# Optimization experiments

Hardware: AMD Instinct MI355X
Metric: run time of the kernel (lower is better)

## Reference

```python
import jax, jax.numpy as jnp
import numpy as np

ITERATIONS = 3
OUT_CAPS, OUT_DIM = 10, 16


def squash(x):
    # square_norm / (1 + square_norm) * x / (sqrt(square_norm) + 1e-6), norm over last axis
    sn = jnp.sum(x * x, axis=-1, keepdims=True)
    return sn / (1.0 + sn) * x / (jnp.sqrt(sn) + 1e-6)


def setup_inputs() -> dict:
    key = jax.random.key(0)
    kx, kw = jax.random.split(key)
    x = jax.random.normal(kx, (256, 32, 6, 6, 8), dtype=jnp.float32)
    W = 0.01 * jax.random.normal(kw, (1, 32, 6, 6, 10, 8, 16), dtype=jnp.float32)
    return {"x": x, "W": W}


def reference(x, W):
    w = W[0]  # [i,j,k,o,d,e]
    # u_hat: prediction vectors, [B, i, j, k, O, E]
    u_hat = jnp.einsum('bijkd,ijkode->bijkoe', x, w)
    u_det = jax.lax.stop_gradient(u_hat)
    b = jnp.zeros(u_hat.shape[:-1], dtype=u_hat.dtype)  # [B,i,j,k,O]
    for _ in range(ITERATIONS - 1):
        c = jax.nn.softmax(b, axis=-1)
        s = jnp.einsum('bijko,bijkoe->boe', c, u_det)   # reduce over all input-capsule axes
        v = squash(s)                                    # [B,O,E]
        b = b + jnp.einsum('bijkoe,boe->bijko', u_det, v)
    c = jax.nn.softmax(b, axis=-1)
    s = jnp.einsum('bijko,bijkoe->boe', c, u_hat)
    v = squash(s)
    return v.reshape(-1, OUT_CAPS, OUT_DIM)
```

## Files before the change

### kernel.cpp

```cpp
#include <hip/hip_runtime.h>
#include <math.h>

#define BATCH 256
#define IC    1152
#define DD    8
#define OO    10
#define EE    16
#define BTILE 64
#define NBT   4
#define NT    256
#define CHUNK 6
#define NCHUNK 192
#define WPC   1280
#define WHALF ((size_t)IC * 160 * 8)

typedef __attribute__((ext_vector_type(8))) short short8;
typedef __attribute__((ext_vector_type(4))) float f32x4;

__device__ __forceinline__ unsigned short f2bf(float f) {
    unsigned u = __float_as_uint(f);
    unsigned r = u + 0x7FFFu + ((u >> 16) & 1u);
    return (unsigned short)(r >> 16);
}
__device__ __forceinline__ float bf2f(unsigned short h) {
    return __uint_as_float(((unsigned)h) << 16);
}

__global__ __launch_bounds__(256) void caps_prep_kernel(
    const float* __restrict__ W,
    unsigned short* __restrict__ w_hi,
    unsigned short* __restrict__ w_lo)
{
    const int idx = blockIdx.x * 256 + threadIdx.x;
    const int ijk = idx / 160;
    const int oe  = idx - ijk * 160;
    const int o = oe >> 4, e = oe & 15;
    const float* src = W + (size_t)ijk * WPC + o * 128 + e;
    short8 hv, lv;
    #pragma unroll
    for (int d = 0; d < 8; ++d) {
        const float f = src[d * 16];
        const unsigned short h = f2bf(f);
        hv[d] = (short)h;
        lv[d] = (short)f2bf(f - bf2f(h));
    }
    *reinterpret_cast<short8*>(w_hi + (size_t)idx * 8) = hv;
    *reinterpret_cast<short8*>(w_lo + (size_t)idx * 8) = lv;
}

__global__ __launch_bounds__(NT) void caps_pass_kernel(
    const float* __restrict__ x,
    const unsigned short* __restrict__ w_hi,
    const unsigned short* __restrict__ w_lo,
    const float* __restrict__ V,
    float* __restrict__ s_part,
    int first)
{
    __shared__ unsigned short wl_hi[CHUNK * 160 * 8];
    __shared__ unsigned short wl_lo[CHUNK * 160 * 8];
    __shared__ unsigned short x_hi[CHUNK][BTILE][8];
    __shared__ unsigned short x_lo[CHUNK][BTILE][8];
    __shared__ unsigned short zpad[8];

    const int tid  = threadIdx.x;
    const int wv   = tid >> 6;
    const int lane = tid & 63;
    const int q    = lane >> 4;
    const int em   = lane & 15;
    const int ijk0 = blockIdx.x * CHUNK;
    const int bg0  = blockIdx.y * BTILE;

    if (tid < 8) zpad[tid] = 0;

    {
        const float4* sh = reinterpret_cast<const float4*>(w_hi + (size_t)ijk0 * 160 * 8);
        const float4* sl = reinterpret_cast<const float4*>(w_lo + (size_t)ijk0 * 160 * 8);
        float4* dh = reinterpret_cast<float4*>(wl_hi);
        float4* dl = reinterpret_cast<float4*>(wl_lo);
        #pragma unroll
        for (int i = 0; i < 4; ++i) {
            const int f = tid + i * NT;
            if (f < CHUNK * 160) { dh[f] = sh[f]; dl[f] = sl[f]; }
        }
    }
    {
        #pragma unroll
        for (int i = 0; i < 2; ++i) {
            const int u = tid + i * NT;
            if (u < CHUNK * BTILE) {
                const int b = u / CHUNK, s = u - b * CHUNK;
                const float* xp = x + ((size_t)(bg0 + b) * IC + (ijk0 + s)) * DD;
                const float4 xa = *reinterpret_cast<const float4*>(xp);
                const float4 xb = *reinterpret_cast<const float4*>(xp + 4);
                const float vv[8] = {xa.x,xa.y,xa.z,xa.w, xb.x,xb.y,xb.z,xb.w};
                short8 hv, lv;
                #pragma unroll
                for (int j = 0; j < 8; ++j) {
                    const unsigned short h = f2bf(vv[j]);
                    hv[j] = (short)h;
                    lv[j] = (short)f2bf(vv[j] - bf2f(h));
                }
                *reinterpret_cast<short8*>(&x_hi[s][b][0]) = hv;
                *reinterpret_cast<short8*>(&x_lo[s][b][0]) = lv;
            }
        }
    }

    f32x4 vreg[OO];
    const int b = bg0 + 16 * wv + em;
    if (!first) {
        #pragma unroll
        for (int o = 0; o < OO; ++o) {
            const float4 t = *reinterpret_cast<const float4*>(
                V + (size_t)b * (OO * EE) + o * EE + 4 * q);
            vreg[o] = (f32x4){t.x, t.y, t.z, t.w};
        }
    }
    __syncthreads();

    const unsigned short* wbase = (q == 1) ? wl_lo : ((q == 3) ? zpad : wl_hi);
    const unsigned short* xbase = (q == 2) ? &x_lo[0][0][0]
                                : ((q == 3) ? zpad : &x_hi[0][0][0]);
    const int msk = (q == 3) ? 0 : 1;

    f32x4 sacc[OO];
    #pragma unroll
    for (int o = 0; o < OO; ++o) sacc[o] = (f32x4){0.f, 0.f, 0.f, 0.f};

    #pragma unroll 1
    for (int s = 0; s < CHUNK; ++s) {
        const short8 xf = *reinterpret_cast<const short8*>(
            xbase + msk * ((s * BTILE + 16 * wv + em) * 8));
        f32x4 u[OO];
        #pragma unroll
        for (int o = 0; o < OO; ++o) {
            const short8 wf = *reinterpret_cast<const short8*>(
                wbase + msk * ((s * 160 + o * 16 + em) * 8));
            u[o] = __builtin_amdgcn_mfma_f32_16x16x32_bf16(
                       wf, xf, (f32x4){0.f, 0.f, 0.f, 0.f}, 0, 0, 0);
        }
        if (!first) {
            float elg[OO];
            float den = 0.f;
            #pragma unroll
            for (int o = 0; o < OO; ++o) {
                float t = u[o][0]*vreg[o][0] + u[o][1]*vreg[o][1]
                        + u[o][2]*vreg[o][2] + u[o][3]*vreg[o][3];
                t += __shfl_xor(t, 16);
                t += __shfl_xor(t, 32);
                elg[o] = __expf(t);
                den += elg[o];
            }
            const float rden = __fdividef(1.0f, den);
            #pragma unroll
            for (int o = 0; o < OO; ++o)
                sacc[o] += u[o] * (elg[o] * rden);
        } else {
            #pragma unroll
            for (int o = 0; o < OO; ++o) sacc[o] += u[o];
        }
    }

    {
        const float mul = first ? 0.1f : 1.0f;
        float* sp = s_part + (((size_t)blockIdx.x * BATCH + b) * OO) * EE + 4 * q;
        #pragma unroll
        for (int o = 0; o < OO; ++o) {
            const f32x4 t = sacc[o];
            float4 w4;
            w4.x = mul * t[0]; w4.y = mul * t[1];
            w4.z = mul * t[2]; w4.w = mul * t[3];
            *reinterpret_cast<float4*>(sp + o * EE) = w4;
        }
    }
}

__global__ __launch_bounds__(1024) void caps_squash_kernel(
    const float* __restrict__ s_part,
    float* __restrict__ V,
    float* __restrict__ out,
    int accum, int last)
{
    __shared__ float red[15][64];
    const int lane = threadIdx.x & 63;
    const int w    = threadIdx.x >> 6;
    const int g    = blockIdx.x * 64 + lane;

    const float* sp = s_part + g;
    float s = 0.f;
    #pragma unroll
    for (int i = 0; i < NCHUNK / 16; ++i)
        s += sp[(size_t)(w * (NCHUNK / 16) + i) * (BATCH * OO * EE)];

    if (w > 0) red[w - 1][lane] = s;
    __syncthreads();
    if (w == 0) {
        #pragma unroll
        for (int i = 0; i < 15; ++i) s += red[i][lane];

        float sq = s * s;
        #pragma unroll
        for (int m = 1; m < 16; m <<= 1) sq += __shfl_xor(sq, m, 16);

        const float scale = sq / (1.f + sq) / (sqrtf(sq) + 1e-6f);
        const float v = scale * s;

        if (last)       out[g] = v;
        else if (accum) V[g]  += v;
        else            V[g]   = v;
    }
}

extern "C" void kernel_launch(void* const* d_in, const int* in_sizes, int n_in,
                              void* d_out, int out_size, void* d_ws, size_t ws_size,
                              hipStream_t stream) {
    const float* x = (const float*)d_in[0];
    const float* W = (const float*)d_in[1];
    float* out = (float*)d_out;

    float* s_part = (float*)d_ws;
    float* V      = s_part + (size_t)NCHUNK * BATCH * OO * EE;
    unsigned short* w_hi = (unsigned short*)(V + BATCH * OO * EE);
    unsigned short* w_lo = w_hi + WHALF;

    dim3 grid(NCHUNK, NBT), blk(NT);
    const int sq_blocks = (BATCH * OO * EE) / 64;

    caps_prep_kernel<<<(IC * 160) / 256, 256, 0, stream>>>(W, w_hi, w_lo);

    caps_pass_kernel<<<grid, blk, 0, stream>>>(x, w_hi, w_lo, V, s_part, 1);
    caps_squash_kernel<<<sq_blocks, 1024, 0, stream>>>(s_part, V, out, 0, 0);
    caps_pass_kernel<<<grid, blk, 0, stream>>>(x, w_hi, w_lo, V, s_part, 0);
    caps_squash_kernel<<<sq_blocks, 1024, 0, stream>>>(s_part, V, out, 1, 0);
    caps_pass_kernel<<<grid, blk, 0, stream>>>(x, w_hi, w_lo, V, s_part, 0);
    caps_squash_kernel<<<sq_blocks, 1024, 0, stream>>>(s_part, V, out, 0, 1);
}
```

Measured before the change: 152.8 us.

## Recompute MFMA predictions instead of holding them; shrink chunk to four capsules

The routing pass no longer keeps all ten u vectors live across the softmax. It recomputes each MFMA product in a second loop, with an opaque copy of the LDS base pointer so the compiler cannot merge the two loads. This cuts register pressure in exchange for twice the MFMA and LDS reads. The input-capsule chunk shrinks from 6 to 4, which gives more blocks, lets the x staging use one element per thread, and shrinks LDS per block, but adds more partial sums for the squash kernel to reduce.

```diff
diff --git a/kernel.cpp b/kernel.cpp
--- a/kernel.cpp
+++ b/kernel.cpp
@@ -9,8 +9,8 @@
 #define BTILE 64
 #define NBT   4
 #define NT    256
-#define CHUNK 6
-#define NCHUNK 192
+#define CHUNK 4
+#define NCHUNK 288
 #define WPC   1280
 #define WHALF ((size_t)IC * 160 * 8)
 
@@ -78,32 +78,26 @@
         float4* dh = reinterpret_cast<float4*>(wl_hi);
         float4* dl = reinterpret_cast<float4*>(wl_lo);
         #pragma unroll
-        for (int i = 0; i < 4; ++i) {
+        for (int i = 0; i < 3; ++i) {
             const int f = tid + i * NT;
             if (f < CHUNK * 160) { dh[f] = sh[f]; dl[f] = sl[f]; }
         }
     }
     {
-        #pragma unroll
-        for (int i = 0; i < 2; ++i) {
-            const int u = tid + i * NT;
-            if (u < CHUNK * BTILE) {
-                const int b = u / CHUNK, s = u - b * CHUNK;
-                const float* xp = x + ((size_t)(bg0 + b) * IC + (ijk0 + s)) * DD;
-                const float4 xa = *reinterpret_cast<const float4*>(xp);
-                const float4 xb = *reinterpret_cast<const float4*>(xp + 4);
-                const float vv[8] = {xa.x,xa.y,xa.z,xa.w, xb.x,xb.y,xb.z,xb.w};
-                short8 hv, lv;
-                #pragma unroll
-                for (int j = 0; j < 8; ++j) {
-                    const unsigned short h = f2bf(vv[j]);
-                    hv[j] = (short)h;
-                    lv[j] = (short)f2bf(vv[j] - bf2f(h));
-                }
-                *reinterpret_cast<short8*>(&x_hi[s][b][0]) = hv;
-                *reinterpret_cast<short8*>(&x_lo[s][b][0]) = lv;
-            }
-        }
+        const int b = tid >> 2, s = tid & 3;
+        const float* xp = x + ((size_t)(bg0 + b) * IC + (ijk0 + s)) * DD;
+        const float4 xa = *reinterpret_cast<const float4*>(xp);
+        const float4 xb = *reinterpret_cast<const float4*>(xp + 4);
+        const float vv[8] = {xa.x,xa.y,xa.z,xa.w, xb.x,xb.y,xb.z,xb.w};
+        short8 hv, lv;
+        #pragma unroll
+        for (int j = 0; j < 8; ++j) {
+            const unsigned short h = f2bf(vv[j]);
+            hv[j] = (short)h;
+            lv[j] = (short)f2bf(vv[j] - bf2f(h));
+        }
+        *reinterpret_cast<short8*>(&x_hi[s][b][0]) = hv;
+        *reinterpret_cast<short8*>(&x_lo[s][b][0]) = lv;
     }
 
     f32x4 vreg[OO];
@@ -123,6 +117,10 @@
                                 : ((q == 3) ? zpad : &x_hi[0][0][0]);
     const int msk = (q == 3) ? 0 : 1;
 
+    uintptr_t wb2i = (uintptr_t)wbase;
+    asm volatile("" : "+v"(wb2i));
+    const unsigned short* wbase2 = (const unsigned short*)wb2i;
+
     f32x4 sacc[OO];
     #pragma unroll
     for (int o = 0; o < OO; ++o) sacc[o] = (f32x4){0.f, 0.f, 0.f, 0.f};
@@ -131,33 +129,43 @@
     for (int s = 0; s < CHUNK; ++s) {
         const short8 xf = *reinterpret_cast<const short8*>(
             xbase + msk * ((s * BTILE + 16 * wv + em) * 8));
-        f32x4 u[OO];
-        #pragma unroll
-        for (int o = 0; o < OO; ++o) {
-            const short8 wf = *reinterpret_cast<const short8*>(
-                wbase + msk * ((s * 160 + o * 16 + em) * 8));
-            u[o] = __builtin_amdgcn_mfma_f32_16x16x32_bf16(
-                       wf, xf, (f32x4){0.f, 0.f, 0.f, 0.f}, 0, 0, 0);
-        }
+        const int woff = (s * 160 + em) * 8;
+
         if (!first) {
             float elg[OO];
-            float den = 0.f;
             #pragma unroll
             for (int o = 0; o < OO; ++o) {
-                float t = u[o][0]*vreg[o][0] + u[o][1]*vreg[o][1]
-                        + u[o][2]*vreg[o][2] + u[o][3]*vreg[o][3];
+                const short8 wf = *reinterpret_cast<const short8*>(
+                    wbase + msk * (woff + o * 128));
+                const f32x4 u = __builtin_amdgcn_mfma_f32_16x16x32_bf16(
+                                    wf, xf, (f32x4){0.f,0.f,0.f,0.f}, 0, 0, 0);
+                float t = u[0]*vreg[o][0] + u[1]*vreg[o][1]
+                        + u[2]*vreg[o][2] + u[3]*vreg[o][3];
                 t += __shfl_xor(t, 16);
                 t += __shfl_xor(t, 32);
                 elg[o] = __expf(t);
-                den += elg[o];
             }
+            const float d01 = elg[0] + elg[1], d23 = elg[2] + elg[3];
+            const float d45 = elg[4] + elg[5], d67 = elg[6] + elg[7];
+            const float den = ((d01 + d23) + (d45 + d67)) + (elg[8] + elg[9]);
             const float rden = __fdividef(1.0f, den);
             #pragma unroll
-            for (int o = 0; o < OO; ++o)
-                sacc[o] += u[o] * (elg[o] * rden);
+            for (int o = 0; o < OO; ++o) {
+                const short8 wf = *reinterpret_cast<const short8*>(
+                    wbase2 + msk * (woff + o * 128));
+                const f32x4 u = __builtin_amdgcn_mfma_f32_16x16x32_bf16(
+                                    wf, xf, (f32x4){0.f,0.f,0.f,0.f}, 0, 0, 0);
+                sacc[o] += u * (elg[o] * rden);
+            }
         } else {
             #pragma unroll
-            for (int o = 0; o < OO; ++o) sacc[o] += u[o];
+            for (int o = 0; o < OO; ++o) {
+                const short8 wf = *reinterpret_cast<const short8*>(
+                    wbase + msk * (woff + o * 128));
+                const f32x4 u = __builtin_amdgcn_mfma_f32_16x16x32_bf16(
+                                    wf, xf, (f32x4){0.f,0.f,0.f,0.f}, 0, 0, 0);
+                sacc[o] += u;
+            }
         }
     }
 
```

Result: slower. 171.7 us (+12.3%).
